# Kernel optimization log

Hardware: AMD Instinct MI355X
Metric: run time of the kernel (lower is better)

Reference implementation:

```python
import jax, jax.numpy as jnp
import numpy as np

B, S, D, H = 2, 2048, 2048, 32
DH = D // H
NEG = -1e9


def setup_inputs() -> dict:
    key = jax.random.key(0)
    ks = jax.random.split(key, 10)
    sc = 0.02
    hidden_state = jax.random.normal(ks[0], (B, S, D), dtype=jnp.float32)
    # additive causal mask, broadcastable to [B,H,S,S]
    causal = jnp.tril(jnp.ones((S, S), dtype=bool))
    mask = jnp.where(causal, 0.0, NEG).astype(jnp.float32)[None, None]
    return {
        "hidden_state": hidden_state,
        "mask": mask,
        "q_w": jax.random.normal(ks[1], (D, D), jnp.float32) * sc,
        "q_b": jnp.zeros((D,), jnp.float32),
        "k_w": jax.random.normal(ks[2], (D, D), jnp.float32) * sc,
        "k_b": jnp.zeros((D,), jnp.float32),
        "v_w": jax.random.normal(ks[3], (D, D), jnp.float32) * sc,
        "v_b": jnp.zeros((D,), jnp.float32),
        "o_w": jax.random.normal(ks[4], (D, D), jnp.float32) * sc,
        "o_b": jnp.zeros((D,), jnp.float32),
    }


def reference(hidden_state, mask, q_w, q_b, k_w, k_b, v_w, v_b, o_w, o_b):
    scale = DH ** -0.5
    # projections (torch Linear: x @ W^T + b)
    q = (hidden_state @ q_w.T + q_b).reshape(B, S, H, DH).transpose(0, 2, 1, 3) * scale
    k = (hidden_state @ k_w.T + k_b).reshape(B, S, H, DH).transpose(0, 2, 1, 3)
    v = (hidden_state @ v_w.T + v_b).reshape(B, S, H, DH).transpose(0, 2, 1, 3)
    qk = jnp.einsum('bhqd,bhkd->bhqk', q, k) + mask
    attn = jax.nn.softmax(qk, axis=-1)
    o = jnp.einsum('bhqk,bhkd->bhqd', attn, v)
    o = o.transpose(0, 2, 1, 3).reshape(B, S, D)
    return o @ o_w.T + o_b
```

## Files before the change

kernel.cpp:

```cpp
#include <hip/hip_runtime.h>
#include <stdint.h>

#define Hh   32
#define Ss   2048
#define Dd   2048
#define DHd  64
#define Mtok 4096
#define MiB  (1u << 20)
#define NTK  32

typedef unsigned short u16;
typedef u16   u16x4  __attribute__((ext_vector_type(4)));
typedef u16   u16x8  __attribute__((ext_vector_type(8)));
typedef short bf16x8 __attribute__((ext_vector_type(8)));
typedef float f32x4  __attribute__((ext_vector_type(4)));

__device__ __forceinline__ u16 f2bf(float f) {
    union { float f; uint32_t u; } v; v.f = f;
    uint32_t r = v.u + 0x7fffu + ((v.u >> 16) & 1u);
    return (u16)(r >> 16);
}
__device__ __forceinline__ uint32_t cvtpk_bf16(float lo, float hi) {
    uint32_t r;
    asm volatile("v_cvt_pk_bf16_f32 %0, %1, %2" : "=v"(r) : "v"(lo), "v"(hi));
    return r;
}
__device__ __forceinline__ void gld_lds16(const void* g, void* l) {
    __builtin_amdgcn_global_load_lds(
        (const __attribute__((address_space(1))) uint32_t*)g,
        (__attribute__((address_space(3))) uint32_t*)l,
        16, 0, 0);
}
#define SB() __builtin_amdgcn_sched_barrier(0)

__global__ void cvt_all(const float* __restrict__ x,  const float* __restrict__ qw,
                        const float* __restrict__ kw, const float* __restrict__ vw,
                        const float* __restrict__ ow,
                        u16* __restrict__ Xb, u16* __restrict__ Wcat, u16* __restrict__ Wob)
{
    const size_t nX = 1u << 23, nW = 1u << 22;
    size_t i = ((size_t)blockIdx.x * 256 + threadIdx.x) * 8;
    const float* src; u16* dst; size_t off;
    if (i < nX) { src = x; dst = Xb; off = i; }
    else {
        size_t j = i - nX;
        int seg = (int)(j >> 22);
        off = j & (nW - 1);
        src = (seg == 0) ? qw : (seg == 1) ? kw : (seg == 2) ? vw : ow;
        dst = (seg == 3) ? Wob : Wcat + (size_t)seg * nW;
    }
    f32x4 a = *(const f32x4*)(src + off);
    f32x4 b = *(const f32x4*)(src + off + 4);
    u16x8 o;
    o[0] = f2bf(a[0]); o[1] = f2bf(a[1]); o[2] = f2bf(a[2]); o[3] = f2bf(a[3]);
    o[4] = f2bf(b[0]); o[5] = f2bf(b[1]); o[6] = f2bf(b[2]); o[7] = f2bf(b[3]);
    *(u16x8*)(dst + off) = o;
}

__device__ __forceinline__ void stage_unitA(const u16* __restrict__ src, u16* dst, int wid, int lane)
{
    const int P = wid * 64 + lane;
    const int rp = P >> 3, c4p = P & 7, c4 = c4p ^ (rp & 7);
    const int r = rp * 2 + (c4 >> 2), c = (c4 & 3) * 8;
    gld_lds16(src + (size_t)r * Dd + c, dst + wid * 512);
}
__device__ __forceinline__ void stage_unitB(const u16* __restrict__ src, u16* dst, int wid, int lane)
{
#pragma unroll
    for (int j = 0; j < 2; ++j) {
        const int P = j * 512 + wid * 64 + lane;
        const int rp = P >> 3, c4p = P & 7, c4 = c4p ^ (rp & 7);
        const int r = rp * 2 + (c4 >> 2), c = (c4 & 3) * 8;
        gld_lds16(src + (size_t)r * Dd + c, dst + j * 4096 + wid * 512);
    }
}
__device__ __forceinline__ bf16x8 frag_read(const u16* unit, int r, int lg)
{
    const int rp = r >> 1;
    const int c4 = ((r & 1) << 2) | lg;
    const int c4p = c4 ^ (rp & 7);
    return *(const bf16x8*)(unit + rp * 64 + c4p * 8);
}

__device__ __forceinline__ void gemm2_core(const u16* __restrict__ Ab, const u16* __restrict__ Wb,
                                           u16* L, f32x4 acc[4][4],
                                           int wid, int lane, int l15, int lg, int wm, int wn)
{
    u16* const L0 = L;
    u16* const L1 = L + 24576;
    stage_unitA(Ab + 0,  L0 + 0,     wid, lane);
    stage_unitB(Wb + 0,  L0 + 8192,  wid, lane);
    stage_unitA(Ab + 32, L0 + 4096,  wid, lane);
    stage_unitB(Wb + 32, L0 + 16384, wid, lane);
    stage_unitA(Ab + 64, L1 + 0,     wid, lane);
    stage_unitB(Wb + 64, L1 + 8192,  wid, lane);
    asm volatile("s_waitcnt vmcnt(6)" ::: "memory");
    SB(); __builtin_amdgcn_s_barrier(); SB();

    const int aro = wm * 64 + l15;
    const int bro = wn * 64 + l15;
#pragma unroll 2
    for (int t = 0; t < NTK; ++t) {
        u16* const Lc = (t & 1) ? L1 : L0;
        u16* const Ln = (t & 1) ? L0 : L1;
#pragma unroll
        for (int ph = 0; ph < 2; ++ph) {
            const u16* Au = Lc + ph * 4096;
            const u16* Bu = Lc + 8192 + ph * 8192;
            bf16x8 bfr[4], a[4];
#pragma unroll
            for (int ni = 0; ni < 4; ++ni) bfr[ni] = frag_read(Bu, bro + ni * 16, lg);
#pragma unroll
            for (int mi = 0; mi < 4; ++mi) a[mi] = frag_read(Au, aro + mi * 16, lg);
            if (ph == 0) {
                if (t + 1 < NTK) {
                    stage_unitA(Ab + (t + 1) * 64 + 32, Ln + 4096,  wid, lane);
                    stage_unitB(Wb + (t + 1) * 64 + 32, Ln + 16384, wid, lane);
                }
            } else {
                if (t + 2 < NTK) {
                    stage_unitA(Ab + (t + 2) * 64, Lc + 0,    wid, lane);
                    stage_unitB(Wb + (t + 2) * 64, Lc + 8192, wid, lane);
                }
            }
            asm volatile("s_waitcnt lgkmcnt(0)" ::: "memory");
            SB();
            __builtin_amdgcn_s_setprio(1);
#pragma unroll
            for (int mi = 0; mi < 4; ++mi)
#pragma unroll
                for (int ni = 0; ni < 4; ++ni)
                    acc[mi][ni] = __builtin_amdgcn_mfma_f32_16x16x32_bf16(a[mi], bfr[ni], acc[mi][ni], 0, 0, 0);
            __builtin_amdgcn_s_setprio(0);
            const bool deep = (ph == 0) ? (t + 1 < NTK) : (t + 2 < NTK);
            if (deep) { asm volatile("s_waitcnt vmcnt(6)" ::: "memory"); }
            else      { asm volatile("s_waitcnt vmcnt(0)" ::: "memory"); }
            SB(); __builtin_amdgcn_s_barrier(); SB();
        }
    }
}

__device__ __forceinline__ void gemm256_core(const u16* __restrict__ Ab, const u16* __restrict__ Wb,
                                             u16* L, f32x4 acc[8][4],
                                             int wid, int lane, int l15, int lg, int wm, int wn)
{
    u16* const L0 = L;
    u16* const L1 = L + 32768;
    stage_unitB(Ab + 0,  L0 + 0,     wid, lane);
    stage_unitB(Wb + 0,  L0 + 16384, wid, lane);
    stage_unitB(Ab + 32, L0 + 8192,  wid, lane);
    stage_unitB(Wb + 32, L0 + 24576, wid, lane);
    stage_unitB(Ab + 64, L1 + 0,     wid, lane);
    stage_unitB(Wb + 64, L1 + 16384, wid, lane);
    asm volatile("s_waitcnt vmcnt(4)" ::: "memory");
    SB(); __builtin_amdgcn_s_barrier(); SB();

    const int arow = wm * 128 + l15;
    const int bro  = wn * 64 + l15;
#pragma unroll 2
    for (int t = 0; t < NTK; ++t) {
        u16* const Lc = (t & 1) ? L1 : L0;
        u16* const Ln = (t & 1) ? L0 : L1;
#pragma unroll
        for (int sp = 0; sp < 2; ++sp) {
            const u16* Au = Lc + sp * 8192;
            const u16* Bu = Lc + 16384 + sp * 8192;
            bf16x8 bfr[4], alo[4], ahi[4];
#pragma unroll
            for (int ni = 0; ni < 4; ++ni) bfr[ni] = frag_read(Bu, bro + ni * 16, lg);
#pragma unroll
            for (int mi = 0; mi < 4; ++mi) alo[mi] = frag_read(Au, arow + mi * 16, lg);
#pragma unroll
            for (int mi = 0; mi < 4; ++mi) ahi[mi] = frag_read(Au, arow + (mi + 4) * 16, lg);
            bool staged;
            if (sp == 0) {
                staged = (t + 1 < NTK);
                if (staged) {
                    stage_unitB(Ab + (t + 1) * 64 + 32, Ln + 8192,  wid, lane);
                    stage_unitB(Wb + (t + 1) * 64 + 32, Ln + 24576, wid, lane);
                }
            } else {
                staged = (t + 2 < NTK);
                if (staged) {
                    stage_unitB(Ab + (t + 2) * 64, Lc + 0,     wid, lane);
                    stage_unitB(Wb + (t + 2) * 64, Lc + 16384, wid, lane);
                }
            }
            asm volatile("s_waitcnt lgkmcnt(4)" ::: "memory");
            SB();
            __builtin_amdgcn_s_setprio(1);
#pragma unroll
            for (int mi = 0; mi < 4; ++mi)
#pragma unroll
                for (int ni = 0; ni < 4; ++ni)
                    acc[mi][ni] = __builtin_amdgcn_mfma_f32_16x16x32_bf16(alo[mi], bfr[ni], acc[mi][ni], 0, 0, 0);
            __builtin_amdgcn_s_setprio(0);
            asm volatile("s_waitcnt lgkmcnt(0)" ::: "memory");
            SB();
            __builtin_amdgcn_s_setprio(1);
#pragma unroll
            for (int mi = 0; mi < 4; ++mi)
#pragma unroll
                for (int ni = 0; ni < 4; ++ni)
                    acc[mi + 4][ni] = __builtin_amdgcn_mfma_f32_16x16x32_bf16(ahi[mi], bfr[ni], acc[mi + 4][ni], 0, 0, 0);
            __builtin_amdgcn_s_setprio(0);
            if (staged) { asm volatile("s_waitcnt vmcnt(4)" ::: "memory"); }
            else        { asm volatile("s_waitcnt vmcnt(0)" ::: "memory"); }
            SB(); __builtin_amdgcn_s_barrier(); SB();
        }
    }
}

__global__ __launch_bounds__(512, 1) void gemm_qkv256(
    const u16* __restrict__ X, const u16* __restrict__ Wcat,
    const float* __restrict__ Bq, const float* __restrict__ Bk, const float* __restrict__ Bv,
    u16* __restrict__ Qo, u16* __restrict__ Ko, u16* __restrict__ Vo)
{
    __shared__ __align__(16) u16 L[2 * 32768];
    const int tid = threadIdx.x, wid = tid >> 6, lane = tid & 63;
    const int l15 = lane & 15, lg = lane >> 4;
    const int wm = wid >> 2, wn = wid & 3;
    const int bid = blockIdx.x;
    const int swz = (bid & 7) * 48 + (bid >> 3);
    const int m0 = (swz / 24) * 256, n0 = (swz % 24) * 256;

    f32x4 acc[8][4] = {};
    gemm256_core(X + (size_t)m0 * Dd, Wcat + (size_t)n0 * Dd, L, acc, wid, lane, l15, lg, wm, wn);

#pragma unroll
    for (int ni = 0; ni < 4; ++ni) {
        const int n = n0 + wn * 64 + ni * 16 + l15;
        const int z = n >> 11, nn = n & 2047;
        const float bv = (z == 0 ? Bq : z == 1 ? Bk : Bv)[nn];
        const float sc = (z == 0) ? 0.125f : 1.0f;
        u16* Out = (z == 0 ? Qo : z == 1 ? Ko : Vo);
        const int h = nn >> 6, dh = nn & 63;
#pragma unroll
        for (int mi = 0; mi < 8; ++mi)
#pragma unroll
            for (int r = 0; r < 4; ++r) {
                const int m = m0 + wm * 128 + mi * 16 + lg * 4 + r;
                const int b = m >> 11, s = m & 2047;
                Out[(((size_t)b * Hh + h) * Ss + s) * DHd + dh] = f2bf((acc[mi][ni][r] + bv) * sc);
            }
    }
}

__global__ __launch_bounds__(512) void gemm_oproj8(
    const u16* __restrict__ A, const u16* __restrict__ W,
    const float* __restrict__ Bi, float* __restrict__ Out)
{
    __shared__ __align__(16) u16 L[2 * 24576];
    const int tid = threadIdx.x, wid = tid >> 6, lane = tid & 63;
    const int l15 = lane & 15, lg = lane >> 4;
    const int wm = wid >> 2, wn = wid & 3;
    const int m0 = blockIdx.x * 128, n0 = blockIdx.y * 256;

    f32x4 acc[4][4] = {};
    gemm2_core(A + (size_t)m0 * Dd, W + (size_t)n0 * Dd, L, acc, wid, lane, l15, lg, wm, wn);

#pragma unroll
    for (int ni = 0; ni < 4; ++ni) {
        const int n = n0 + wn * 64 + ni * 16 + l15;
        const float bv = Bi[n];
#pragma unroll
        for (int mi = 0; mi < 4; ++mi)
#pragma unroll
            for (int r = 0; r < 4; ++r) {
                const int m = m0 + wm * 64 + mi * 16 + lg * 4 + r;
                Out[(size_t)m * Dd + n] = acc[mi][ni][r] + bv;
            }
    }
}

__global__ void transpose_v(const u16* __restrict__ Vsrc, u16* __restrict__ Vdst)
{
    __shared__ __align__(16) u16 t[64 * 68];
    const int bh = blockIdx.y, s0 = blockIdx.x * 64;
    const int tid = threadIdx.x;
    {
        const int r = tid >> 2, cq = (tid & 3) * 16;
        const u16* src = Vsrc + ((size_t)bh * Ss + s0 + r) * DHd;
#pragma unroll
        for (int j = 0; j < 4; ++j) {
            u16x4 v = *(const u16x4*)(src + cq + j * 4);
            *(u16x4*)&t[r * 68 + cq + j * 4] = v;
        }
    }
    __syncthreads();
    {
        const int d = tid >> 2, sq = (tid & 3) * 16;
        u16* dst = Vdst + ((size_t)bh * DHd + d) * Ss + s0;
#pragma unroll
        for (int j = 0; j < 4; ++j) {
            u16x4 v;
            v.x = t[(sq + j * 4 + 0) * 68 + d];
            v.y = t[(sq + j * 4 + 1) * 68 + d];
            v.z = t[(sq + j * 4 + 2) * 68 + d];
            v.w = t[(sq + j * 4 + 3) * 68 + d];
            *(u16x4*)(dst + sq + j * 4) = v;
        }
    }
}

__device__ __forceinline__ void stage_kv(const u16* __restrict__ Kg, const u16* __restrict__ Vg,
                                         u16* Kl, u16* Vl, int kv0, int tid)
{
    const int u    = tid;
    const int row  = u >> 3;
    const int csrc = ((u & 7) ^ (row & 7)) * 8;
    const int base = (u & ~63) * 8;
    gld_lds16(Kg + (size_t)(kv0 + row) * DHd + csrc, Kl + base);
    gld_lds16(Vg + (size_t)row * Ss + kv0 + csrc, Vl + base);
}

__device__ __forceinline__ void attn_tile(
    const u16* __restrict__ Kc, const u16* __restrict__ Vc, int kv0,
    int q0, int qrow, int l15, int lg, int psw,
    const bf16x8* __restrict__ bq, f32x4* __restrict__ o,
    float& m_r, float& l_r, char* __restrict__ prow)
{
    if (kv0 > q0 + 15) return;
    f32x4 s[4] = {};
    __builtin_amdgcn_s_setprio(1);
#pragma unroll
    for (int nb = 0; nb < 4; ++nb) {
        const int krow = nb * 16 + l15;
        const char* rb = (const char*)(Kc + krow * 64);
        const int sw = (krow & 7) << 4;
#pragma unroll
        for (int kf = 0; kf < 2; ++kf) {
            bf16x8 ak = *(const bf16x8*)(rb + ((kf * 64 + lg * 16) ^ sw));
            s[nb] = __builtin_amdgcn_mfma_f32_16x16x32_bf16(ak, bq[kf], s[nb], 0, 0, 0);
        }
    }
    __builtin_amdgcn_s_setprio(0);
    if (kv0 + 63 > q0) {
#pragma unroll
        for (int nb = 0; nb < 4; ++nb)
#pragma unroll
            for (int r = 0; r < 4; ++r)
                if (kv0 + nb * 16 + lg * 4 + r > qrow) s[nb][r] = -3e38f;
    }
    float pm = -3e38f;
#pragma unroll
    for (int nb = 0; nb < 4; ++nb)
#pragma unroll
        for (int r = 0; r < 4; ++r) pm = fmaxf(pm, s[nb][r]);
    pm = fmaxf(pm, __shfl_xor(pm, 16, 64));
    pm = fmaxf(pm, __shfl_xor(pm, 32, 64));
    const bool full = !__all(pm - m_r <= 8.0f);
    float mn = m_r, al = 1.0f;
    if (full) {
        mn = fmaxf(m_r, pm);
        al = __expf(m_r - mn);
#pragma unroll
        for (int nb = 0; nb < 4; ++nb)
#pragma unroll
            for (int r = 0; r < 4; ++r) o[nb][r] *= al;
    }
    float rs = 0.f;
    float p[4][4];
#pragma unroll
    for (int nb = 0; nb < 4; ++nb)
#pragma unroll
        for (int r = 0; r < 4; ++r) { p[nb][r] = __expf(s[nb][r] - mn); rs += p[nb][r]; }
    rs += __shfl_xor(rs, 16, 64);
    rs += __shfl_xor(rs, 32, 64);
    l_r = l_r * al + rs;
    m_r = mn;
#pragma unroll
    for (int nb = 0; nb < 4; ++nb) {
        const uint32_t w0 = cvtpk_bf16(p[nb][0], p[nb][1]);
        const uint32_t w1 = cvtpk_bf16(p[nb][2], p[nb][3]);
        const int c0 = (nb * 32 + lg * 8) ^ psw;
        *(uint32_t*)(prow + c0)     = w0;
        *(uint32_t*)(prow + c0 + 4) = w1;
    }
    bf16x8 pa[2];
#pragma unroll
    for (int ks = 0; ks < 2; ++ks)
        pa[ks] = *(const bf16x8*)(prow + ((ks * 64 + lg * 16) ^ psw));
    __builtin_amdgcn_s_setprio(1);
#pragma unroll
    for (int nb = 0; nb < 4; ++nb) {
        const int vrow = nb * 16 + l15;
        const char* rb = (const char*)(Vc + vrow * 64);
        const int sw = (vrow & 7) << 4;
#pragma unroll
        for (int ks = 0; ks < 2; ++ks) {
            bf16x8 bv = *(const bf16x8*)(rb + ((ks * 64 + lg * 16) ^ sw));
            o[nb] = __builtin_amdgcn_mfma_f32_16x16x32_bf16(bv, pa[ks], o[nb], 0, 0, 0);
        }
    }
    __builtin_amdgcn_s_setprio(0);
}

__global__ __launch_bounds__(512) void attn(
    const u16* __restrict__ Qb, const u16* __restrict__ Kb,
    const u16* __restrict__ Vt, u16* __restrict__ Ob)
{
    __shared__ __align__(16) u16 Kl[2][4096];
    __shared__ __align__(16) u16 Vl[2][4096];
    __shared__ __align__(16) u16 PlA[8][1024];
    __shared__ __align__(16) u16 PlB[8][1024];
    const int bh = blockIdx.y;
    const int b = bh >> 5, h = bh & 31;
    const int tid = threadIdx.x;
    const int wid = tid >> 6, lane = tid & 63;
    const int l15 = lane & 15, lg = lane >> 4;
    const int bxA = blockIdx.x, bxB = 15 - bxA;
    const int q0A = bxA * 128 + wid * 16, q0B = bxB * 128 + wid * 16;
    const int qrowA = q0A + l15, qrowB = q0B + l15;
    char* prowA = (char*)PlA[wid] + l15 * 128;
    char* prowB = (char*)PlB[wid] + l15 * 128;
    const int psw = (l15 & 7) << 4;

    const u16* Kp = Kb + (size_t)bh * Ss * DHd;
    const u16* Vp = Vt + (size_t)bh * DHd * Ss;

    bf16x8 bqA[2], bqB[2];
    {
        const u16* QpA = Qb + ((size_t)bh * Ss + q0A) * DHd;
        const u16* QpB = Qb + ((size_t)bh * Ss + q0B) * DHd;
#pragma unroll
        for (int kf = 0; kf < 2; ++kf) {
            bqA[kf] = *(const bf16x8*)(QpA + (size_t)l15 * DHd + kf * 32 + lg * 8);
            bqB[kf] = *(const bf16x8*)(QpB + (size_t)l15 * DHd + kf * 32 + lg * 8);
        }
    }
    asm volatile("s_waitcnt vmcnt(0)" ::: "memory");

    f32x4 oA[4] = {}, oB[4] = {};
    float mA = -3e38f, lA = 0.f, mB = -3e38f, lB = 0.f;
    const int nt = 2 * (bxB + 1);

    stage_kv(Kp, Vp, Kl[0], Vl[0], 0, tid);
    for (int t = 0; t < nt; ++t) {
        if (t + 1 < nt) {
            stage_kv(Kp, Vp, Kl[(t + 1) & 1], Vl[(t + 1) & 1], (t + 1) * 64, tid);
            asm volatile("s_waitcnt vmcnt(2)" ::: "memory");
        } else {
            asm volatile("s_waitcnt vmcnt(0)" ::: "memory");
        }
        SB(); __builtin_amdgcn_s_barrier(); SB();
        const int kv0 = t * 64;
        attn_tile(Kl[t & 1], Vl[t & 1], kv0, q0A, qrowA, l15, lg, psw, bqA, oA, mA, lA, prowA);
        attn_tile(Kl[t & 1], Vl[t & 1], kv0, q0B, qrowB, l15, lg, psw, bqB, oB, mB, lB, prowB);
        SB(); __builtin_amdgcn_s_barrier(); SB();
    }

    {
        const float inv = 1.0f / lA;
        u16* orow = Ob + ((size_t)b * Ss + qrowA) * Dd + h * DHd;
#pragma unroll
        for (int nb = 0; nb < 4; ++nb) {
            u16x4 pk;
#pragma unroll
            for (int r = 0; r < 4; ++r) pk[r] = f2bf(oA[nb][r] * inv);
            *(u16x4*)(orow + nb * 16 + lg * 4) = pk;
        }
    }
    {
        const float inv = 1.0f / lB;
        u16* orow = Ob + ((size_t)b * Ss + qrowB) * Dd + h * DHd;
#pragma unroll
        for (int nb = 0; nb < 4; ++nb) {
            u16x4 pk;
#pragma unroll
            for (int r = 0; r < 4; ++r) pk[r] = f2bf(oB[nb][r] * inv);
            *(u16x4*)(orow + nb * 16 + lg * 4) = pk;
        }
    }
}

extern "C" void kernel_launch(void* const* d_in, const int* in_sizes, int n_in,
                              void* d_out, int out_size, void* d_ws, size_t ws_size,
                              hipStream_t stream)
{
    (void)in_sizes; (void)n_in; (void)out_size; (void)ws_size;
    const float* x  = (const float*)d_in[0];
    const float* qw = (const float*)d_in[2];
    const float* qb = (const float*)d_in[3];
    const float* kw = (const float*)d_in[4];
    const float* kb = (const float*)d_in[5];
    const float* vw = (const float*)d_in[6];
    const float* vb = (const float*)d_in[7];
    const float* ow = (const float*)d_in[8];
    const float* obias = (const float*)d_in[9];

    uint8_t* ws = (uint8_t*)d_ws;
    u16* Xb  = (u16*)(ws);
    u16* Wcat= (u16*)(ws + 16 * MiB);
    u16* Wob = (u16*)(ws + 40 * MiB);
    u16* Qb  = (u16*)(ws + 48 * MiB);
    u16* Kb  = (u16*)(ws + 64 * MiB);
    u16* Vb  = (u16*)(ws + 80 * MiB);
    u16* Vt  = Xb;
    u16* Ob  = Vb;

    cvt_all<<<12288, 256, 0, stream>>>(x, qw, kw, vw, ow, Xb, Wcat, Wob);

    gemm_qkv256<<<384, 512, 0, stream>>>(Xb, Wcat, qb, kb, vb, Qb, Kb, Vb);
    transpose_v<<<dim3(Ss / 64, 64), dim3(256), 0, stream>>>(Vb, Vt);
    attn<<<dim3(8, 64), dim3(512), 0, stream>>>(Qb, Kb, Vt, Ob);
    gemm_oproj8<<<dim3(Mtok / 128, Dd / 256), dim3(512), 0, stream>>>(
        Ob, Wob, obias, (float*)d_out);
}
```

Before: 257.9 us.

## Use 16 waves per block in QKV GEMM with 64x64 per-wave tiles

```diff
diff --git a/kernel.cpp b/kernel.cpp
--- a/kernel.cpp
+++ b/kernel.cpp
@@ -72,6 +72,20 @@
         const int rp = P >> 3, c4p = P & 7, c4 = c4p ^ (rp & 7);
         const int r = rp * 2 + (c4 >> 2), c = (c4 & 3) * 8;
         gld_lds16(src + (size_t)r * Dd + c, dst + j * 4096 + wid * 512);
+    }
+}
+__device__ __forceinline__ void stage_pair16(const u16* __restrict__ Asrc, const u16* __restrict__ Bsrc,
+                                             u16* Adst, u16* Bdst, int wid, int lane)
+{
+    const int uid = wid & 7;
+    const u16* src = (wid < 8) ? Asrc : Bsrc;
+    u16*       dst = (wid < 8) ? Adst : Bdst;
+#pragma unroll
+    for (int j = 0; j < 2; ++j) {
+        const int P = j * 512 + uid * 64 + lane;
+        const int rp = P >> 3, c4p = P & 7, c4 = c4p ^ (rp & 7);
+        const int r = rp * 2 + (c4 >> 2), c = (c4 & 3) * 8;
+        gld_lds16(src + (size_t)r * Dd + c, dst + j * 4096 + uid * 512);
     }
 }
 __device__ __forceinline__ bf16x8 frag_read(const u16* unit, int r, int lg)
@@ -140,23 +154,20 @@
     }
 }
 
-__device__ __forceinline__ void gemm256_core(const u16* __restrict__ Ab, const u16* __restrict__ Wb,
-                                             u16* L, f32x4 acc[8][4],
-                                             int wid, int lane, int l15, int lg, int wm, int wn)
+__device__ __forceinline__ void gemm256w16_core(const u16* __restrict__ Ab, const u16* __restrict__ Wb,
+                                                u16* L, f32x4 acc[4][4],
+                                                int wid, int lane, int l15, int lg, int wm, int wn)
 {
     u16* const L0 = L;
     u16* const L1 = L + 32768;
-    stage_unitB(Ab + 0,  L0 + 0,     wid, lane);
-    stage_unitB(Wb + 0,  L0 + 16384, wid, lane);
-    stage_unitB(Ab + 32, L0 + 8192,  wid, lane);
-    stage_unitB(Wb + 32, L0 + 24576, wid, lane);
-    stage_unitB(Ab + 64, L1 + 0,     wid, lane);
-    stage_unitB(Wb + 64, L1 + 16384, wid, lane);
-    asm volatile("s_waitcnt vmcnt(4)" ::: "memory");
+    stage_pair16(Ab + 0,  Wb + 0,  L0 + 0,    L0 + 16384, wid, lane);
+    stage_pair16(Ab + 32, Wb + 32, L0 + 8192, L0 + 24576, wid, lane);
+    stage_pair16(Ab + 64, Wb + 64, L1 + 0,    L1 + 16384, wid, lane);
+    asm volatile("s_waitcnt vmcnt(2)" ::: "memory");
     SB(); __builtin_amdgcn_s_barrier(); SB();
 
-    const int arow = wm * 128 + l15;
-    const int bro  = wn * 64 + l15;
+    const int aro = wm * 64 + l15;
+    const int bro = wn * 64 + l15;
 #pragma unroll 2
     for (int t = 0; t < NTK; ++t) {
         u16* const Lc = (t & 1) ? L1 : L0;
@@ -165,36 +176,21 @@
         for (int sp = 0; sp < 2; ++sp) {
             const u16* Au = Lc + sp * 8192;
             const u16* Bu = Lc + 16384 + sp * 8192;
-            bf16x8 bfr[4], alo[4], ahi[4];
+            bf16x8 bfr[4], a[4];
 #pragma unroll
             for (int ni = 0; ni < 4; ++ni) bfr[ni] = frag_read(Bu, bro + ni * 16, lg);
 #pragma unroll
-            for (int mi = 0; mi < 4; ++mi) alo[mi] = frag_read(Au, arow + mi * 16, lg);
-#pragma unroll
-            for (int mi = 0; mi < 4; ++mi) ahi[mi] = frag_read(Au, arow + (mi + 4) * 16, lg);
+            for (int mi = 0; mi < 4; ++mi) a[mi] = frag_read(Au, aro + mi * 16, lg);
             bool staged;
             if (sp == 0) {
                 staged = (t + 1 < NTK);
-                if (staged) {
-                    stage_unitB(Ab + (t + 1) * 64 + 32, Ln + 8192,  wid, lane);
-                    stage_unitB(Wb + (t + 1) * 64 + 32, Ln + 24576, wid, lane);
-                }
+                if (staged) stage_pair16(Ab + (t + 1) * 64 + 32, Wb + (t + 1) * 64 + 32,
+                                         Ln + 8192, Ln + 24576, wid, lane);
             } else {
                 staged = (t + 2 < NTK);
-                if (staged) {
-                    stage_unitB(Ab + (t + 2) * 64, Lc + 0,     wid, lane);
-                    stage_unitB(Wb + (t + 2) * 64, Lc + 16384, wid, lane);
-                }
+                if (staged) stage_pair16(Ab + (t + 2) * 64, Wb + (t + 2) * 64,
+                                         Lc + 0, Lc + 16384, wid, lane);
             }
-            asm volatile("s_waitcnt lgkmcnt(4)" ::: "memory");
-            SB();
-            __builtin_amdgcn_s_setprio(1);
-#pragma unroll
-            for (int mi = 0; mi < 4; ++mi)
-#pragma unroll
-                for (int ni = 0; ni < 4; ++ni)
-                    acc[mi][ni] = __builtin_amdgcn_mfma_f32_16x16x32_bf16(alo[mi], bfr[ni], acc[mi][ni], 0, 0, 0);
-            __builtin_amdgcn_s_setprio(0);
             asm volatile("s_waitcnt lgkmcnt(0)" ::: "memory");
             SB();
             __builtin_amdgcn_s_setprio(1);
@@ -202,7 +198,7 @@
             for (int mi = 0; mi < 4; ++mi)
 #pragma unroll
                 for (int ni = 0; ni < 4; ++ni)
-                    acc[mi + 4][ni] = __builtin_amdgcn_mfma_f32_16x16x32_bf16(ahi[mi], bfr[ni], acc[mi + 4][ni], 0, 0, 0);
+                    acc[mi][ni] = __builtin_amdgcn_mfma_f32_16x16x32_bf16(a[mi], bfr[ni], acc[mi][ni], 0, 0, 0);
             __builtin_amdgcn_s_setprio(0);
             if (staged) { asm volatile("s_waitcnt vmcnt(4)" ::: "memory"); }
             else        { asm volatile("s_waitcnt vmcnt(0)" ::: "memory"); }
@@ -211,7 +207,7 @@
     }
 }
 
-__global__ __launch_bounds__(512, 1) void gemm_qkv256(
+__global__ __launch_bounds__(1024, 1) void gemm_qkv256(
     const u16* __restrict__ X, const u16* __restrict__ Wcat,
     const float* __restrict__ Bq, const float* __restrict__ Bk, const float* __restrict__ Bv,
     u16* __restrict__ Qo, u16* __restrict__ Ko, u16* __restrict__ Vo)
@@ -224,8 +220,8 @@
     const int swz = (bid & 7) * 48 + (bid >> 3);
     const int m0 = (swz / 24) * 256, n0 = (swz % 24) * 256;
 
-    f32x4 acc[8][4] = {};
-    gemm256_core(X + (size_t)m0 * Dd, Wcat + (size_t)n0 * Dd, L, acc, wid, lane, l15, lg, wm, wn);
+    f32x4 acc[4][4] = {};
+    gemm256w16_core(X + (size_t)m0 * Dd, Wcat + (size_t)n0 * Dd, L, acc, wid, lane, l15, lg, wm, wn);
 
 #pragma unroll
     for (int ni = 0; ni < 4; ++ni) {
@@ -236,10 +232,10 @@
         u16* Out = (z == 0 ? Qo : z == 1 ? Ko : Vo);
         const int h = nn >> 6, dh = nn & 63;
 #pragma unroll
-        for (int mi = 0; mi < 8; ++mi)
+        for (int mi = 0; mi < 4; ++mi)
 #pragma unroll
             for (int r = 0; r < 4; ++r) {
-                const int m = m0 + wm * 128 + mi * 16 + lg * 4 + r;
+                const int m = m0 + wm * 64 + mi * 16 + lg * 4 + r;
                 const int b = m >> 11, s = m & 2047;
                 Out[(((size_t)b * Hh + h) * Ss + s) * DHd + dh] = f2bf((acc[mi][ni][r] + bv) * sc);
             }
@@ -501,7 +497,7 @@
 
     cvt_all<<<12288, 256, 0, stream>>>(x, qw, kw, vw, ow, Xb, Wcat, Wob);
 
-    gemm_qkv256<<<384, 512, 0, stream>>>(Xb, Wcat, qb, kb, vb, Qb, Kb, Vb);
+    gemm_qkv256<<<384, 1024, 0, stream>>>(Xb, Wcat, qb, kb, vb, Qb, Kb, Vb);
     transpose_v<<<dim3(Ss / 64, 64), dim3(256), 0, stream>>>(Vb, Vt);
     attn<<<dim3(8, 64), dim3(512), 0, stream>>>(Qb, Kb, Vt, Ob);
     gemm_oproj8<<<dim3(Mtok / 128, Dd / 256), dim3(512), 0, stream>>>(
```

Measured after the change: 299.3 us. +16.0%, slower.
